# Optimization experiments

Hardware: AMD Instinct MI355X
Metric: run time of the kernel (lower is better)

## Reference

```python
import jax, jax.numpy as jnp
import numpy as np

B, L, D, F, E = 64, 512, 512, 2048, 8
EPS = 1e-9

def setup_inputs() -> dict:
    key = jax.random.key(0)
    ks = jax.random.split(key, 8)
    x = jax.random.normal(ks[0], (B, L, D), dtype=jnp.float32)
    logits = jax.random.normal(ks[1], (B, E), dtype=jnp.float32)
    moe_masks = jax.random.randint(ks[2], (B, E), 0, 2, dtype=jnp.int32)
    # per-expert MLP params: Linear(D->F), GELU, Linear(F->D)
    w1 = jax.random.normal(ks[3], (E, D, F), dtype=jnp.float32) / np.sqrt(D)
    b1 = jnp.zeros((E, F), dtype=jnp.float32)
    w2 = jax.random.normal(ks[4], (E, F, D), dtype=jnp.float32) / np.sqrt(F)
    b2 = jnp.zeros((E, D), dtype=jnp.float32)
    return {"cycle_curve_data": x, "logits": logits, "moe_masks": moe_masks,
            "w1": w1, "b1": b1, "w2": w2, "b2": b2}

def reference(cycle_curve_data, logits, moe_masks, w1, b1, w2, b2):
    x = cycle_curve_data
    mask = (moe_masks == 1).astype(logits.dtype)           # [B,E]
    raw = jax.nn.softmax(logits, axis=1)                   # [B,E]
    gated = raw * mask
    gates = gated / (jnp.sum(gated, axis=1, keepdims=True) + EPS)  # renormalized [B,E]
    # dispatch/combine: combine == sum_e gates[:,e] * expert_e(x); zero-gate rows
    # contribute nothing, matching the index-based dispatcher exactly.
    out = jnp.zeros_like(x)
    n_exp = w1.shape[0]
    for e in range(n_exp):
        h = jax.nn.gelu(jnp.einsum('bld,df->blf', x, w1[e]) + b1[e], approximate=False)
        y = jnp.einsum('blf,fd->bld', h, w2[e]) + b2[e]
        out = out + gates[:, e, None, None] * y
    bsz = x.shape[0]
    guide_loss = (1.0 - jnp.sum(raw * mask) / bsz) ** 2
    return out, guide_loss
```

## Files before the change

kernel.cpp:

```cpp
#include <hip/hip_runtime.h>
#include <math.h>

#define Bb 64
#define Ll 512
#define Dd 512
#define Ff 2048
#define Ee 8

typedef _Float16 half_t;
typedef _Float16 half8 __attribute__((ext_vector_type(8)));
typedef float f32x4 __attribute__((ext_vector_type(4)));

#define W2T_OFF ((size_t)Ee * Dd * Ff)

__device__ __forceinline__ void dma16(const half_t* g, half_t* l) {
    __builtin_amdgcn_global_load_lds((const __attribute__((address_space(1))) void*)g,
                                     (__attribute__((address_space(3))) void*)l, 16, 0, 0);
}
__device__ __forceinline__ void dma16f(const float* g, float* l) {
    __builtin_amdgcn_global_load_lds((const __attribute__((address_space(1))) void*)g,
                                     (__attribute__((address_space(3))) void*)l, 16, 0, 0);
}

#define VWAIT(n)  asm volatile("s_waitcnt vmcnt(" #n ")" ::: "memory")
#define VLWAIT(n) asm volatile("s_waitcnt vmcnt(" #n ") lgkmcnt(0)" ::: "memory")
#define BAR() do { __builtin_amdgcn_s_barrier();                 \
                   asm volatile("" ::: "memory");                \
                   __builtin_amdgcn_sched_barrier(0); } while (0)

__global__ __launch_bounds__(256)
void prep_transpose(const float* __restrict__ w1, const float* __restrict__ w2,
                    half_t* __restrict__ ws)
{
    __shared__ half_t T[64 * 72];
    int bid = blockIdx.x;
    const float* src; half_t* dst; int R, C, r0, c0;
    if (bid < 2048) {
        int e = bid >> 8, t = bid & 255;
        r0 = (t >> 5) * 64; c0 = (t & 31) * 64;
        src = w1 + (size_t)e * Dd * Ff;
        dst = ws + (size_t)e * Ff * Dd;
        R = Dd; C = Ff;
    } else {
        bid -= 2048;
        int e = bid >> 8, t = bid & 255;
        r0 = (t >> 3) * 64; c0 = (t & 7) * 64;
        src = w2 + (size_t)e * Ff * Dd;
        dst = ws + W2T_OFF + (size_t)e * Dd * Ff;
        R = Ff; C = Dd;
    }
    const int cx = threadIdx.x & 63, ry = threadIdx.x >> 6;
    #pragma unroll
    for (int j = 0; j < 16; ++j) {
        int r = ry * 16 + j;
        T[cx * 72 + r] = (half_t)src[(size_t)(r0 + r) * C + c0 + cx];
    }
    __syncthreads();
    const int rx = threadIdx.x & 7;
    #pragma unroll
    for (int it = 0; it < 2; ++it) {
        int cr = (threadIdx.x >> 3) + it * 32;
        *(half8*)&dst[(size_t)(c0 + cr) * R + r0 + rx * 8] = *(half8*)&T[cr * 72 + rx * 8];
    }
}

__global__ __launch_bounds__(512, 2)
void moe_main(const float* __restrict__ x, const float* __restrict__ logits,
              const int* __restrict__ masks, const half_t* __restrict__ ws,
              const float* __restrict__ b1, const float* __restrict__ b2,
              float* __restrict__ out)
{
    __shared__ half_t Wbuf[3][128 * 128];
    __shared__ half_t Hs[64 * 128];
    __shared__ float  Bs[128];

    const int tid  = threadIdx.x;
    const int wv   = tid >> 6;
    const int lane = tid & 63;
    const int nl   = lane & 15;
    const int q    = lane >> 4;
    const int mt   = wv >> 1;
    const int nh   = wv & 1;
    const int rl   = lane >> 4;
    const int pcl  = lane & 15;

    const int bid = blockIdx.x;

    int b;
    {
        int cj = 0;
        #pragma unroll
        for (int e2 = 0; e2 < Ee; ++e2) cj += (masks[lane * Ee + e2] == 1);
        int rj = 0;
        for (int k = 0; k < Bb; ++k) {
            const int ck = __shfl(cj, k);
            rj += (ck > cj) || (ck == cj && k < lane);
        }
        const unsigned long long mword = __ballot(rj == (bid >> 3));
        b = (int)__builtin_ctzll(mword);
    }
    const int l0 = (bid & 7) * 64;

    float mx = -1e30f;
    #pragma unroll
    for (int e = 0; e < Ee; ++e) mx = fmaxf(mx, logits[b * Ee + e]);
    float s = 0.f, gs = 0.f;
    unsigned am = 0u;
    #pragma unroll
    for (int e = 0; e < Ee; ++e) {
        const float ex = expf(logits[b * Ee + e] - mx);
        s += ex;
        if (masks[b * Ee + e] == 1) { gs += ex; am |= (1u << e); }
    }
    const int el = lane & 7;
    const float myg = ((am >> el) & 1u)
        ? expf(logits[b * Ee + el] - mx) / (gs + 1e-9f * s) : 0.f;
    float ge[Ee];
    #pragma unroll
    for (int e = 0; e < Ee; ++e) ge[e] = __shfl(myg, e);

    half8 afrag[16];
    {
        const float* xrow = x + (size_t)(b * Ll + l0 + mt * 16 + nl) * Dd;
        #pragma unroll
        for (int ks = 0; ks < 16; ++ks) {
            const int c0 = ks * 32 + q * 8;
            const f32x4 u0 = *(const f32x4*)(xrow + c0);
            const f32x4 u1 = *(const f32x4*)(xrow + c0 + 4);
            half8 a;
            a[0]=(half_t)u0[0]; a[1]=(half_t)u0[1]; a[2]=(half_t)u0[2]; a[3]=(half_t)u0[3];
            a[4]=(half_t)u1[0]; a[5]=(half_t)u1[1]; a[6]=(half_t)u1[2]; a[7]=(half_t)u1[3];
            afrag[ks] = a;
        }
    }

    f32x4 oacc[16];
    #pragma unroll
    for (int i = 0; i < 16; ++i) oacc[i] = (f32x4){0.f, 0.f, 0.f, 0.f};

    auto stageT = [&](const half_t* src, int ld, half_t* dst) {
        #pragma unroll
        for (int ss = 0; ss < 4; ++ss) {
            const int row = wv * 16 + ss * 4 + rl;
            const int c = pcl ^ (row & 15);
            dma16(src + (size_t)row * ld + c * 8, dst + (wv * 16 + ss * 4) * 128);
        }
    };
    auto computeA = [&](const half8* af, const half_t* Wb, f32x4* hc) {
        #pragma unroll
        for (int ks = 0; ks < 4; ++ks) {
            const half8 a = af[ks];
            #pragma unroll
            for (int nf = 0; nf < 4; ++nf) {
                const int row = nh * 64 + nf * 16 + nl;
                const half8 bf = *(const half8*)&Wb[row * 128 + (((ks * 4 + q) ^ nl) * 8)];
                hc[nf] = __builtin_amdgcn_mfma_f32_16x16x32_f16(a, bf, hc[nf], 0, 0, 0);
            }
        }
    };
    auto computeB = [&](const half8* ha, const half_t* Wb, f32x4* oc) {
        #pragma unroll
        for (int ks = 0; ks < 4; ++ks) {
            #pragma unroll
            for (int t = 0; t < 4; ++t) {
                const int lr = t * 32 + nh * 16 + nl;
                const half8 bf = *(const half8*)&Wb[lr * 128 + (((ks * 4 + q) ^ nl) * 8)];
                oc[t] = __builtin_amdgcn_mfma_f32_16x16x32_f16(ha[ks], bf, oc[t], 0, 0, 0);
            }
        }
    };

    int cur = 0;
    unsigned rem = am;
    if (rem) {
        const int e0 = (int)__builtin_ctz(rem);
        const half_t* W1p = ws + (size_t)e0 * Ff * Dd;
        asm volatile("s_waitcnt vmcnt(0)" ::: "memory");
        stageT(W1p,       Dd, Wbuf[0]);
        if (lane < 32) dma16f(b1 + (size_t)e0 * Ff + lane * 4, Bs);
        stageT(W1p + 128, Dd, Wbuf[1]);
        VWAIT(4);
        BAR();
    }

    while (rem) {
        const int e = (int)__builtin_ctz(rem); rem &= rem - 1u;
        const int en = rem ? (int)__builtin_ctz(rem) : -1;
        const float g = __shfl(myg, e);
        const half_t* W1te = ws + (size_t)e * Ff * Dd;
        const half_t* W2te = ws + W2T_OFF + (size_t)e * Dd * Ff;
        const half_t* W1nx = (en >= 0) ? ws + (size_t)en * Ff * Dd : W1te;
        const float*  b1nx = (en >= 0) ? b1 + (size_t)en * Ff : b1;

        #pragma unroll 1
        for (int fci = 0; fci < 16; ++fci) {
            const int f0 = fci * 128;
            const half_t* WA = W1te + (size_t)f0 * Dd;
            const half_t* WB = W2te + f0;
            const bool hn = (fci < 15) || (en >= 0);
            const half_t* An = (fci < 15) ? (WA + (size_t)128 * Dd) : W1nx;
            const float*  bn = (fci < 15) ? (b1 + (size_t)e * Ff + f0 + 128) : b1nx;

            f32x4 hacc[4];
            #pragma unroll
            for (int i = 0; i < 4; ++i) hacc[i] = (f32x4){0.f, 0.f, 0.f, 0.f};

            { half_t* Wp = Wbuf[cur ? cur - 1 : 2];
              stageT(WA + 2 * 128, Dd, Wp);
              computeA(&afrag[0], Wbuf[cur], hacc);
              VWAIT(4); BAR(); cur = (cur == 2) ? 0 : cur + 1; }
            { half_t* Wp = Wbuf[cur ? cur - 1 : 2];
              stageT(WA + 3 * 128, Dd, Wp);
              computeA(&afrag[4], Wbuf[cur], hacc);
              VWAIT(4); BAR(); cur = (cur == 2) ? 0 : cur + 1; }
            { half_t* Wp = Wbuf[cur ? cur - 1 : 2];
              stageT(WB, Ff, Wp);
              computeA(&afrag[8], Wbuf[cur], hacc);
              VWAIT(4); BAR(); cur = (cur == 2) ? 0 : cur + 1; }
            { half_t* Wp = Wbuf[cur ? cur - 1 : 2];
              stageT(WB + (size_t)128 * Ff, Ff, Wp);
              computeA(&afrag[12], Wbuf[cur], hacc);
              #pragma unroll
              for (int nf = 0; nf < 4; ++nf) {
                  const int fl = nh * 64 + nf * 16 + nl;
                  const float bv = Bs[fl];
                  #pragma unroll
                  for (int r = 0; r < 4; ++r) {
                      const int m = mt * 16 + q * 4 + r;
                      const float v  = hacc[nf][r] + bv;
                      const float gl = 0.5f * v * (1.f + erff(v * 0.70710678118654752f));
                      const int blk = (fl >> 3) ^ (m & 15);
                      Hs[m * 128 + blk * 8 + (fl & 7)] = (half_t)(g * gl);
                  }
              }
              VLWAIT(4); BAR(); cur = (cur == 2) ? 0 : cur + 1; }

            half8 ha[4];
            { half_t* Wp = Wbuf[cur ? cur - 1 : 2];
              #pragma unroll
              for (int ks = 0; ks < 4; ++ks)
                  ha[ks] = *(const half8*)&Hs[(mt * 16 + nl) * 128 + (((ks * 4 + q) ^ nl) * 8)];
              stageT(WB + (size_t)256 * Ff, Ff, Wp);
              computeB(ha, Wbuf[cur], &oacc[0]);
              VWAIT(4); BAR(); cur = (cur == 2) ? 0 : cur + 1; }
            { half_t* Wp = Wbuf[cur ? cur - 1 : 2];
              stageT(WB + (size_t)384 * Ff, Ff, Wp);
              computeB(ha, Wbuf[cur], &oacc[4]);
              VWAIT(4); BAR(); cur = (cur == 2) ? 0 : cur + 1; }
            { half_t* Wp = Wbuf[cur ? cur - 1 : 2];
              if (hn) {
                  stageT(An, Dd, Wp);
                  if (lane < 32) dma16f(bn + lane * 4, Bs);
              }
              computeB(ha, Wbuf[cur], &oacc[8]);
              if (hn) { VWAIT(5); } else { VWAIT(0); }
              BAR(); cur = (cur == 2) ? 0 : cur + 1; }
            { half_t* Wp = Wbuf[cur ? cur - 1 : 2];
              if (hn) stageT(An + 128, Dd, Wp);
              computeB(ha, Wbuf[cur], &oacc[12]);
              if (hn) { VWAIT(4); } else { VWAIT(0); }
              BAR(); cur = (cur == 2) ? 0 : cur + 1; }
        }
    }

    #pragma unroll
    for (int ncc = 0; ncc < 4; ++ncc) {
        #pragma unroll
        for (int t = 0; t < 4; ++t) {
            const int dcol = ncc * 128 + t * 32 + nh * 16 + nl;
            float bb = 0.f;
            #pragma unroll
            for (int e = 0; e < Ee; ++e) bb += ge[e] * b2[e * Dd + dcol];
            const f32x4 v = oacc[ncc * 4 + t];
            const size_t base = (size_t)(b * Ll + l0 + mt * 16 + q * 4) * Dd + dcol;
            out[base]          = v[0] + bb;
            out[base + Dd]     = v[1] + bb;
            out[base + 2 * Dd] = v[2] + bb;
            out[base + 3 * Dd] = v[3] + bb;
        }
    }
}

__global__ void moe_loss(const float* __restrict__ logits, const int* __restrict__ masks,
                         float* __restrict__ loss_out)
{
    const int b = threadIdx.x;
    float lg[Ee];
    float mx = -1e30f;
    #pragma unroll
    for (int e = 0; e < Ee; ++e) { lg[e] = logits[b * Ee + e]; mx = fmaxf(mx, lg[e]); }
    float s = 0.f;
    #pragma unroll
    for (int e = 0; e < Ee; ++e) { float ex = expf(lg[e] - mx); s += ex; lg[e] = ex; }
    float rs = 0.f;
    #pragma unroll
    for (int e = 0; e < Ee; ++e) if (masks[b * Ee + e] == 1) rs += lg[e] / s;
    #pragma unroll
    for (int off = 32; off > 0; off >>= 1) rs += __shfl_down(rs, off);
    if (b == 0) {
        const float t = 1.f - rs / (float)Bb;
        loss_out[0] = t * t;
    }
}

extern "C" void kernel_launch(void* const* d_in, const int* in_sizes, int n_in,
                              void* d_out, int out_size, void* d_ws, size_t ws_size,
                              hipStream_t stream)
{
    const float* x      = (const float*)d_in[0];
    const float* logits = (const float*)d_in[1];
    const int*   masks  = (const int*)d_in[2];
    const float* w1     = (const float*)d_in[3];
    const float* b1     = (const float*)d_in[4];
    const float* w2     = (const float*)d_in[5];
    const float* b2     = (const float*)d_in[6];
    float* out = (float*)d_out;
    half_t* ws = (half_t*)d_ws;

    hipLaunchKernelGGL(prep_transpose, dim3(4096), dim3(256), 0, stream, w1, w2, ws);
    hipLaunchKernelGGL(moe_main, dim3(512), dim3(512), 0, stream,
                       x, logits, masks, ws, b1, b2, out);
    hipLaunchKernelGGL(moe_loss, dim3(1), dim3(64), 0, stream,
                       logits, masks, out + (size_t)Bb * Ll * Dd);
}
```

Before: 1.623 ms.

## Retile waves to 2x4 grid and stream pre-packed fp16 x fragments per chunk

The 8 waves are remapped from a 4x2 (M x N) grid to a 2x4 grid, so each wave now covers 32 rows and 32 columns. Each LDS weight fragment read then feeds two MFMAs instead of one, cutting LDS read traffic per MFMA. The 16 persistent x fragments held in registers are replaced by double-buffered 8-fragment loads that stream from a new fp16 copy of x, pre-packed in MFMA fragment order by an extra xprep kernel. This frees registers, but it adds a conversion kernel over x, more global loads per F-chunk, and adjusted vmcnt waits.

```diff
diff --git a/kernel.cpp b/kernel.cpp
--- a/kernel.cpp
+++ b/kernel.cpp
@@ -12,6 +12,7 @@
 typedef float f32x4 __attribute__((ext_vector_type(4)));
 
 #define W2T_OFF ((size_t)Ee * Dd * Ff)
+#define XH_OFF  ((size_t)2 * Ee * Dd * Ff)
 
 __device__ __forceinline__ void dma16(const half_t* g, half_t* l) {
     __builtin_amdgcn_global_load_lds((const __attribute__((address_space(1))) void*)g,
@@ -24,6 +25,7 @@
 
 #define VWAIT(n)  asm volatile("s_waitcnt vmcnt(" #n ")" ::: "memory")
 #define VLWAIT(n) asm volatile("s_waitcnt vmcnt(" #n ") lgkmcnt(0)" ::: "memory")
+#define SB() __builtin_amdgcn_sched_barrier(0)
 #define BAR() do { __builtin_amdgcn_s_barrier();                 \
                    asm volatile("" ::: "memory");                \
                    __builtin_amdgcn_sched_barrier(0); } while (0)
@@ -64,8 +66,30 @@
     }
 }
 
+__global__ __launch_bounds__(256)
+void xprep(const float* __restrict__ x, half_t* __restrict__ ws)
+{
+    const size_t i = (size_t)blockIdx.x * 256 + threadIdx.x;
+    const int grp = (int)(i & 63);
+    const size_t blk = i >> 6;
+    const int ksg = (int)(blk & 15);
+    const size_t btg = blk >> 4;
+    const int tg = (int)(btg & 31);
+    const int b  = (int)(btg >> 5);
+    const int nl = grp & 15, q = grp >> 4;
+    const int token = tg * 16 + nl;
+    const int k0 = ksg * 32 + q * 8;
+    const float* src = x + (size_t)(b * Ll + token) * Dd + k0;
+    const f32x4 u0 = *(const f32x4*)src;
+    const f32x4 u1 = *(const f32x4*)(src + 4);
+    half8 h;
+    h[0]=(half_t)u0[0]; h[1]=(half_t)u0[1]; h[2]=(half_t)u0[2]; h[3]=(half_t)u0[3];
+    h[4]=(half_t)u1[0]; h[5]=(half_t)u1[1]; h[6]=(half_t)u1[2]; h[7]=(half_t)u1[3];
+    *(half8*)&ws[XH_OFF + i * 8] = h;
+}
+
 __global__ __launch_bounds__(512, 2)
-void moe_main(const float* __restrict__ x, const float* __restrict__ logits,
+void moe_main(const float* __restrict__ logits,
               const int* __restrict__ masks, const half_t* __restrict__ ws,
               const float* __restrict__ b1, const float* __restrict__ b2,
               float* __restrict__ out)
@@ -79,12 +103,14 @@
     const int lane = tid & 63;
     const int nl   = lane & 15;
     const int q    = lane >> 4;
-    const int mt   = wv >> 1;
-    const int nh   = wv & 1;
+    const int mw   = wv >> 2;
+    const int nw   = wv & 3;
     const int rl   = lane >> 4;
     const int pcl  = lane & 15;
 
     const int bid = blockIdx.x;
+    const int rk  = bid >> 3;
+    const int l0  = (bid & 7) * 64;
 
     int b;
     {
@@ -96,10 +122,9 @@
             const int ck = __shfl(cj, k);
             rj += (ck > cj) || (ck == cj && k < lane);
         }
-        const unsigned long long mword = __ballot(rj == (bid >> 3));
+        const unsigned long long mword = __ballot(rj == rk);
         b = (int)__builtin_ctzll(mword);
     }
-    const int l0 = (bid & 7) * 64;
 
     float mx = -1e30f;
     #pragma unroll
@@ -119,20 +144,17 @@
     #pragma unroll
     for (int e = 0; e < Ee; ++e) ge[e] = __shfl(myg, e);
 
-    half8 afrag[16];
-    {
-        const float* xrow = x + (size_t)(b * Ll + l0 + mt * 16 + nl) * Dd;
-        #pragma unroll
-        for (int ks = 0; ks < 16; ++ks) {
-            const int c0 = ks * 32 + q * 8;
-            const f32x4 u0 = *(const f32x4*)(xrow + c0);
-            const f32x4 u1 = *(const f32x4*)(xrow + c0 + 4);
-            half8 a;
-            a[0]=(half_t)u0[0]; a[1]=(half_t)u0[1]; a[2]=(half_t)u0[2]; a[3]=(half_t)u0[3];
-            a[4]=(half_t)u1[0]; a[5]=(half_t)u1[1]; a[6]=(half_t)u1[2]; a[7]=(half_t)u1[3];
-            afrag[ks] = a;
-        }
-    }
+    const half_t* xbase = ws + XH_OFF
+        + ((size_t)(b * 32 + (l0 >> 4) + mw * 2) * 16) * 512 + lane * 8;
+
+    half8 aregA[8], aregB[8];
+    auto aload = [&](int kc, half8* dst) {
+        #pragma unroll
+        for (int ma = 0; ma < 2; ++ma)
+            #pragma unroll
+            for (int ks = 0; ks < 4; ++ks)
+                dst[ma * 4 + ks] = *(const half8*)(xbase + ma * 8192 + (kc * 4 + ks) * 512);
+    };
 
     f32x4 oacc[16];
     #pragma unroll
@@ -146,15 +168,15 @@
             dma16(src + (size_t)row * ld + c * 8, dst + (wv * 16 + ss * 4) * 128);
         }
     };
-    auto computeA = [&](const half8* af, const half_t* Wb, f32x4* hc) {
+    auto computeA = [&](const half8* ar, const half_t* Wb, f32x4* hc) {
         #pragma unroll
         for (int ks = 0; ks < 4; ++ks) {
-            const half8 a = af[ks];
-            #pragma unroll
-            for (int nf = 0; nf < 4; ++nf) {
-                const int row = nh * 64 + nf * 16 + nl;
+            #pragma unroll
+            for (int nf = 0; nf < 2; ++nf) {
+                const int row = nw * 32 + nf * 16 + nl;
                 const half8 bf = *(const half8*)&Wb[row * 128 + (((ks * 4 + q) ^ nl) * 8)];
-                hc[nf] = __builtin_amdgcn_mfma_f32_16x16x32_f16(a, bf, hc[nf], 0, 0, 0);
+                hc[0 + nf] = __builtin_amdgcn_mfma_f32_16x16x32_f16(ar[ks],     bf, hc[0 + nf], 0, 0, 0);
+                hc[2 + nf] = __builtin_amdgcn_mfma_f32_16x16x32_f16(ar[4 + ks], bf, hc[2 + nf], 0, 0, 0);
             }
         }
     };
@@ -162,10 +184,11 @@
         #pragma unroll
         for (int ks = 0; ks < 4; ++ks) {
             #pragma unroll
-            for (int t = 0; t < 4; ++t) {
-                const int lr = t * 32 + nh * 16 + nl;
+            for (int t = 0; t < 2; ++t) {
+                const int lr = nw * 32 + t * 16 + nl;
                 const half8 bf = *(const half8*)&Wb[lr * 128 + (((ks * 4 + q) ^ nl) * 8)];
-                oc[t] = __builtin_amdgcn_mfma_f32_16x16x32_f16(ha[ks], bf, oc[t], 0, 0, 0);
+                oc[0 + t] = __builtin_amdgcn_mfma_f32_16x16x32_f16(ha[ks],     bf, oc[0 + t], 0, 0, 0);
+                oc[2 + t] = __builtin_amdgcn_mfma_f32_16x16x32_f16(ha[4 + ks], bf, oc[2 + t], 0, 0, 0);
             }
         }
     };
@@ -179,7 +202,8 @@
         stageT(W1p,       Dd, Wbuf[0]);
         if (lane < 32) dma16f(b1 + (size_t)e0 * Ff + lane * 4, Bs);
         stageT(W1p + 128, Dd, Wbuf[1]);
-        VWAIT(4);
+        SB(); aload(0, aregA); SB();
+        VWAIT(12);
         BAR();
     }
 
@@ -207,39 +231,47 @@
 
             { half_t* Wp = Wbuf[cur ? cur - 1 : 2];
               stageT(WA + 2 * 128, Dd, Wp);
-              computeA(&afrag[0], Wbuf[cur], hacc);
-              VWAIT(4); BAR(); cur = (cur == 2) ? 0 : cur + 1; }
+              SB(); aload(1, aregB); SB();
+              computeA(aregA, Wbuf[cur], hacc);
+              VWAIT(12); BAR(); cur = (cur == 2) ? 0 : cur + 1; }
             { half_t* Wp = Wbuf[cur ? cur - 1 : 2];
               stageT(WA + 3 * 128, Dd, Wp);
-              computeA(&afrag[4], Wbuf[cur], hacc);
-              VWAIT(4); BAR(); cur = (cur == 2) ? 0 : cur + 1; }
+              SB(); aload(2, aregA); SB();
+              computeA(aregB, Wbuf[cur], hacc);
+              VWAIT(12); BAR(); cur = (cur == 2) ? 0 : cur + 1; }
             { half_t* Wp = Wbuf[cur ? cur - 1 : 2];
               stageT(WB, Ff, Wp);
-              computeA(&afrag[8], Wbuf[cur], hacc);
-              VWAIT(4); BAR(); cur = (cur == 2) ? 0 : cur + 1; }
+              SB(); aload(3, aregB); SB();
+              computeA(aregA, Wbuf[cur], hacc);
+              VWAIT(12); BAR(); cur = (cur == 2) ? 0 : cur + 1; }
             { half_t* Wp = Wbuf[cur ? cur - 1 : 2];
               stageT(WB + (size_t)128 * Ff, Ff, Wp);
-              computeA(&afrag[12], Wbuf[cur], hacc);
+              computeA(aregB, Wbuf[cur], hacc);
               #pragma unroll
-              for (int nf = 0; nf < 4; ++nf) {
-                  const int fl = nh * 64 + nf * 16 + nl;
-                  const float bv = Bs[fl];
+              for (int ma = 0; ma < 2; ++ma)
                   #pragma unroll
-                  for (int r = 0; r < 4; ++r) {
-                      const int m = mt * 16 + q * 4 + r;
-                      const float v  = hacc[nf][r] + bv;
-                      const float gl = 0.5f * v * (1.f + erff(v * 0.70710678118654752f));
-                      const int blk = (fl >> 3) ^ (m & 15);
-                      Hs[m * 128 + blk * 8 + (fl & 7)] = (half_t)(g * gl);
+                  for (int nf = 0; nf < 2; ++nf) {
+                      const int fl = nw * 32 + nf * 16 + nl;
+                      const float bv = Bs[fl];
+                      #pragma unroll
+                      for (int r = 0; r < 4; ++r) {
+                          const int m = mw * 32 + ma * 16 + q * 4 + r;
+                          const float v  = hacc[ma * 2 + nf][r] + bv;
+                          const float gl = 0.5f * v * (1.f + erff(v * 0.70710678118654752f));
+                          const int blk = (fl >> 3) ^ (m & 15);
+                          Hs[m * 128 + blk * 8 + (fl & 7)] = (half_t)(g * gl);
+                      }
                   }
-              }
               VLWAIT(4); BAR(); cur = (cur == 2) ? 0 : cur + 1; }
 
-            half8 ha[4];
+            half8 ha[8];
             { half_t* Wp = Wbuf[cur ? cur - 1 : 2];
               #pragma unroll
-              for (int ks = 0; ks < 4; ++ks)
-                  ha[ks] = *(const half8*)&Hs[(mt * 16 + nl) * 128 + (((ks * 4 + q) ^ nl) * 8)];
+              for (int ma = 0; ma < 2; ++ma)
+                  #pragma unroll
+                  for (int ks = 0; ks < 4; ++ks)
+                      ha[ma * 4 + ks] = *(const half8*)&Hs[(mw * 32 + ma * 16 + nl) * 128
+                                                           + (((ks * 4 + q) ^ nl) * 8)];
               stageT(WB + (size_t)256 * Ff, Ff, Wp);
               computeB(ha, Wbuf[cur], &oacc[0]);
               VWAIT(4); BAR(); cur = (cur == 2) ? 0 : cur + 1; }
@@ -256,9 +288,12 @@
               if (hn) { VWAIT(5); } else { VWAIT(0); }
               BAR(); cur = (cur == 2) ? 0 : cur + 1; }
             { half_t* Wp = Wbuf[cur ? cur - 1 : 2];
-              if (hn) stageT(An + 128, Dd, Wp);
+              if (hn) {
+                  stageT(An + 128, Dd, Wp);
+                  SB(); aload(0, aregA); SB();
+              }
               computeB(ha, Wbuf[cur], &oacc[12]);
-              if (hn) { VWAIT(4); } else { VWAIT(0); }
+              if (hn) { VWAIT(12); } else { VWAIT(0); }
               BAR(); cur = (cur == 2) ? 0 : cur + 1; }
         }
     }
@@ -266,18 +301,20 @@
     #pragma unroll
     for (int ncc = 0; ncc < 4; ++ncc) {
         #pragma unroll
-        for (int t = 0; t < 4; ++t) {
-            const int dcol = ncc * 128 + t * 32 + nh * 16 + nl;
-            float bb = 0.f;
-            #pragma unroll
-            for (int e = 0; e < Ee; ++e) bb += ge[e] * b2[e * Dd + dcol];
-            const f32x4 v = oacc[ncc * 4 + t];
-            const size_t base = (size_t)(b * Ll + l0 + mt * 16 + q * 4) * Dd + dcol;
-            out[base]          = v[0] + bb;
-            out[base + Dd]     = v[1] + bb;
-            out[base + 2 * Dd] = v[2] + bb;
-            out[base + 3 * Dd] = v[3] + bb;
-        }
+        for (int ma = 0; ma < 2; ++ma)
+            #pragma unroll
+            for (int t = 0; t < 2; ++t) {
+                const int dcol = ncc * 128 + nw * 32 + t * 16 + nl;
+                float bb = 0.f;
+                #pragma unroll
+                for (int e = 0; e < Ee; ++e) bb += ge[e] * b2[e * Dd + dcol];
+                const f32x4 v = oacc[ncc * 4 + ma * 2 + t];
+                const size_t base = (size_t)(b * Ll + l0 + mw * 32 + ma * 16 + q * 4) * Dd + dcol;
+                out[base]          = v[0] + bb;
+                out[base + Dd]     = v[1] + bb;
+                out[base + 2 * Dd] = v[2] + bb;
+                out[base + 3 * Dd] = v[3] + bb;
+            }
     }
 }
 
@@ -318,8 +355,9 @@
     half_t* ws = (half_t*)d_ws;
 
     hipLaunchKernelGGL(prep_transpose, dim3(4096), dim3(256), 0, stream, w1, w2, ws);
+    hipLaunchKernelGGL(xprep, dim3(8192), dim3(256), 0, stream, x, ws);
     hipLaunchKernelGGL(moe_main, dim3(512), dim3(512), 0, stream,
-                       x, logits, masks, ws, b1, b2, out);
+                       logits, masks, ws, b1, b2, out);
     hipLaunchKernelGGL(moe_loss, dim3(1), dim3(64), 0, stream,
                        logits, masks, out + (size_t)Bb * Ll * Dd);
 }
```

Measured after the change: 2.336 ms. +43.9%, slower.

## Replace triple-buffered single-tile pipeline with double-buffered two-tile stages

Applied to the files above, without the earlier changes.

Restructures the weight staging pipeline from a 3-slot ring of 128x128 tiles with one tile per barrier step to two buffer pairs, each stage loading two tiles and computing on two. This halves the number of barriers and waits per F-chunk, cutting synchronisation overhead. The cost is full vmcnt(0) waits instead of partial ones, less fine-grained overlap, and more LDS (4 tiles instead of 3), which could reduce occupancy at 2 blocks per CU.

```diff
diff --git a/kernel.cpp b/kernel.cpp
--- a/kernel.cpp
+++ b/kernel.cpp
@@ -22,8 +22,8 @@
                                      (__attribute__((address_space(3))) void*)l, 16, 0, 0);
 }
 
-#define VWAIT(n)  asm volatile("s_waitcnt vmcnt(" #n ")" ::: "memory")
-#define VLWAIT(n) asm volatile("s_waitcnt vmcnt(" #n ") lgkmcnt(0)" ::: "memory")
+#define VWAIT0()  asm volatile("s_waitcnt vmcnt(0)" ::: "memory")
+#define VLWAIT0() asm volatile("s_waitcnt vmcnt(0) lgkmcnt(0)" ::: "memory")
 #define BAR() do { __builtin_amdgcn_s_barrier();                 \
                    asm volatile("" ::: "memory");                \
                    __builtin_amdgcn_sched_barrier(0); } while (0)
@@ -70,7 +70,7 @@
               const float* __restrict__ b1, const float* __restrict__ b2,
               float* __restrict__ out)
 {
-    __shared__ half_t Wbuf[3][128 * 128];
+    __shared__ half_t Wbuf[2][2][128 * 128];
     __shared__ half_t Hs[64 * 128];
     __shared__ float  Bs[128];
 
@@ -85,6 +85,8 @@
     const int pcl  = lane & 15;
 
     const int bid = blockIdx.x;
+    const int rk  = bid >> 3;
+    const int l0  = (bid & 7) * 64;
 
     int b;
     {
@@ -96,10 +98,9 @@
             const int ck = __shfl(cj, k);
             rj += (ck > cj) || (ck == cj && k < lane);
         }
-        const unsigned long long mword = __ballot(rj == (bid >> 3));
+        const unsigned long long mword = __ballot(rj == rk);
         b = (int)__builtin_ctzll(mword);
     }
-    const int l0 = (bid & 7) * 64;
 
     float mx = -1e30f;
     #pragma unroll
@@ -170,16 +171,14 @@
         }
     };
 
-    int cur = 0;
     unsigned rem = am;
     if (rem) {
         const int e0 = (int)__builtin_ctz(rem);
         const half_t* W1p = ws + (size_t)e0 * Ff * Dd;
-        asm volatile("s_waitcnt vmcnt(0)" ::: "memory");
-        stageT(W1p,       Dd, Wbuf[0]);
+        stageT(W1p,       Dd, Wbuf[0][0]);
+        stageT(W1p + 128, Dd, Wbuf[0][1]);
         if (lane < 32) dma16f(b1 + (size_t)e0 * Ff + lane * 4, Bs);
-        stageT(W1p + 128, Dd, Wbuf[1]);
-        VWAIT(4);
+        VWAIT0();
         BAR();
     }
 
@@ -205,61 +204,49 @@
             #pragma unroll
             for (int i = 0; i < 4; ++i) hacc[i] = (f32x4){0.f, 0.f, 0.f, 0.f};
 
-            { half_t* Wp = Wbuf[cur ? cur - 1 : 2];
-              stageT(WA + 2 * 128, Dd, Wp);
-              computeA(&afrag[0], Wbuf[cur], hacc);
-              VWAIT(4); BAR(); cur = (cur == 2) ? 0 : cur + 1; }
-            { half_t* Wp = Wbuf[cur ? cur - 1 : 2];
-              stageT(WA + 3 * 128, Dd, Wp);
-              computeA(&afrag[4], Wbuf[cur], hacc);
-              VWAIT(4); BAR(); cur = (cur == 2) ? 0 : cur + 1; }
-            { half_t* Wp = Wbuf[cur ? cur - 1 : 2];
-              stageT(WB, Ff, Wp);
-              computeA(&afrag[8], Wbuf[cur], hacc);
-              VWAIT(4); BAR(); cur = (cur == 2) ? 0 : cur + 1; }
-            { half_t* Wp = Wbuf[cur ? cur - 1 : 2];
-              stageT(WB + (size_t)128 * Ff, Ff, Wp);
-              computeA(&afrag[12], Wbuf[cur], hacc);
-              #pragma unroll
-              for (int nf = 0; nf < 4; ++nf) {
-                  const int fl = nh * 64 + nf * 16 + nl;
-                  const float bv = Bs[fl];
-                  #pragma unroll
-                  for (int r = 0; r < 4; ++r) {
-                      const int m = mt * 16 + q * 4 + r;
-                      const float v  = hacc[nf][r] + bv;
-                      const float gl = 0.5f * v * (1.f + erff(v * 0.70710678118654752f));
-                      const int blk = (fl >> 3) ^ (m & 15);
-                      Hs[m * 128 + blk * 8 + (fl & 7)] = (half_t)(g * gl);
-                  }
-              }
-              VLWAIT(4); BAR(); cur = (cur == 2) ? 0 : cur + 1; }
-
+            stageT(WA + 2 * 128, Dd, Wbuf[1][0]);
+            stageT(WA + 3 * 128, Dd, Wbuf[1][1]);
+            computeA(&afrag[0], Wbuf[0][0], hacc);
+            computeA(&afrag[4], Wbuf[0][1], hacc);
+            VWAIT0(); BAR();
+
+            stageT(WB,                  Ff, Wbuf[0][0]);
+            stageT(WB + (size_t)128 * Ff, Ff, Wbuf[0][1]);
+            computeA(&afrag[8],  Wbuf[1][0], hacc);
+            computeA(&afrag[12], Wbuf[1][1], hacc);
+            #pragma unroll
+            for (int nf = 0; nf < 4; ++nf) {
+                const int fl = nh * 64 + nf * 16 + nl;
+                const float bv = Bs[fl];
+                #pragma unroll
+                for (int r = 0; r < 4; ++r) {
+                    const int m = mt * 16 + q * 4 + r;
+                    const float v  = hacc[nf][r] + bv;
+                    const float gl = 0.5f * v * (1.f + erff(v * 0.70710678118654752f));
+                    const int blk = (fl >> 3) ^ (m & 15);
+                    Hs[m * 128 + blk * 8 + (fl & 7)] = (half_t)(g * gl);
+                }
+            }
+            VLWAIT0(); BAR();
+
+            stageT(WB + (size_t)256 * Ff, Ff, Wbuf[1][0]);
+            stageT(WB + (size_t)384 * Ff, Ff, Wbuf[1][1]);
             half8 ha[4];
-            { half_t* Wp = Wbuf[cur ? cur - 1 : 2];
-              #pragma unroll
-              for (int ks = 0; ks < 4; ++ks)
-                  ha[ks] = *(const half8*)&Hs[(mt * 16 + nl) * 128 + (((ks * 4 + q) ^ nl) * 8)];
-              stageT(WB + (size_t)256 * Ff, Ff, Wp);
-              computeB(ha, Wbuf[cur], &oacc[0]);
-              VWAIT(4); BAR(); cur = (cur == 2) ? 0 : cur + 1; }
-            { half_t* Wp = Wbuf[cur ? cur - 1 : 2];
-              stageT(WB + (size_t)384 * Ff, Ff, Wp);
-              computeB(ha, Wbuf[cur], &oacc[4]);
-              VWAIT(4); BAR(); cur = (cur == 2) ? 0 : cur + 1; }
-            { half_t* Wp = Wbuf[cur ? cur - 1 : 2];
-              if (hn) {
-                  stageT(An, Dd, Wp);
-                  if (lane < 32) dma16f(bn + lane * 4, Bs);
-              }
-              computeB(ha, Wbuf[cur], &oacc[8]);
-              if (hn) { VWAIT(5); } else { VWAIT(0); }
-              BAR(); cur = (cur == 2) ? 0 : cur + 1; }
-            { half_t* Wp = Wbuf[cur ? cur - 1 : 2];
-              if (hn) stageT(An + 128, Dd, Wp);
-              computeB(ha, Wbuf[cur], &oacc[12]);
-              if (hn) { VWAIT(4); } else { VWAIT(0); }
-              BAR(); cur = (cur == 2) ? 0 : cur + 1; }
+            #pragma unroll
+            for (int ks = 0; ks < 4; ++ks)
+                ha[ks] = *(const half8*)&Hs[(mt * 16 + nl) * 128 + (((ks * 4 + q) ^ nl) * 8)];
+            computeB(ha, Wbuf[0][0], &oacc[0]);
+            computeB(ha, Wbuf[0][1], &oacc[4]);
+            VWAIT0(); BAR();
+
+            if (hn) {
+                stageT(An,       Dd, Wbuf[0][0]);
+                stageT(An + 128, Dd, Wbuf[0][1]);
+                if (lane < 32) dma16f(bn + lane * 4, Bs);
+            }
+            computeB(ha, Wbuf[1][0], &oacc[8]);
+            computeB(ha, Wbuf[1][1], &oacc[12]);
+            VWAIT0(); BAR();
         }
     }
 
```

Result: slower. 2.471 ms (+52.2%).
